# Performance work log

Hardware: AMD Instinct MI355X
Metric: run time of the kernel (lower is better)

Reference implementation:

```python
import jax, jax.numpy as jnp
import numpy as np

B, S, D, H = 2, 2048, 1024, 16
DK = D // H  # 64
ROPE_BASE = 10000.0


def _rope_tables(dk, seq_len, base=ROPE_BASE):
    inv_freq = 1.0 / base ** (jnp.arange(0, dk, 2, dtype=jnp.float32) / dk)
    t = jnp.arange(seq_len, dtype=jnp.float32)
    freqs = t[:, None] * inv_freq[None, :]            # [S, dk/2]
    cos = jnp.repeat(jnp.cos(freqs), 2, axis=-1)      # [S, dk] (repeat_interleave)
    sin = jnp.repeat(jnp.sin(freqs), 2, axis=-1)
    return cos, sin


def _rotate_half(x):
    x1, x2 = jnp.split(x, 2, axis=-1)
    return jnp.concatenate((-x2, x1), axis=-1)


def setup_inputs() -> dict:
    key = jax.random.key(0)
    ks = jax.random.split(key, 9)
    scale = 0.02
    x = jax.random.normal(ks[0], (B, S, D), jnp.float32)
    wq = jax.random.normal(ks[1], (D, D), jnp.float32) * scale
    wk = jax.random.normal(ks[2], (D, D), jnp.float32) * scale
    wv = jax.random.normal(ks[3], (D, D), jnp.float32) * scale
    wo = jax.random.normal(ks[4], (D, D), jnp.float32) * scale
    bq = jnp.zeros((D,), jnp.float32)
    bk = jnp.zeros((D,), jnp.float32)
    bv = jnp.zeros((D,), jnp.float32)
    bo = jnp.zeros((D,), jnp.float32)
    mask = jnp.tril(jnp.ones((S, S), dtype=bool))[None, None]  # [1,1,S,S] causal
    return {"x": x, "mask": mask, "wq": wq, "bq": bq, "wk": wk, "bk": bk,
            "wv": wv, "bv": bv, "wo": wo, "bo": bo}


def reference(x, mask, wq, bq, wk, bk, wv, bv, wo, bo):
    b, s, d = x.shape
    h, dk = H, DK
    # QKV projections (nn.Linear: x @ W^T + b), split heads -> [B,H,S,dk]
    q = (x @ wq.T + bq).reshape(b, s, h, dk).transpose(0, 2, 1, 3)
    k = (x @ wk.T + bk).reshape(b, s, h, dk).transpose(0, 2, 1, 3)
    v = (x @ wv.T + bv).reshape(b, s, h, dk).transpose(0, 2, 1, 3)
    # RoPE
    cos, sin = _rope_tables(dk, s)                    # [S, dk]
    cos = cos[None, None]                             # [1,1,S,dk]
    sin = sin[None, None]
    q = q * cos + _rotate_half(q) * sin
    k = k * cos + _rotate_half(k) * sin
    # Naive attention: full [B,H,S,S] scores
    scores = jnp.einsum("bhqd,bhkd->bhqk", q, k) / np.float32(np.sqrt(dk))
    scores = jnp.where(mask, scores, jnp.float32(-1e9))
    attn = jax.nn.softmax(scores, axis=-1)
    out = jnp.einsum("bhqk,bhkd->bhqd", attn, v)      # [B,H,S,dk]
    out = out.transpose(0, 2, 1, 3).reshape(b, s, d)  # [B,S,D]
    return out @ wo.T + bo
```

## Files before the change

### kernel.cpp

```cpp
#include <hip/hip_runtime.h>
#include <hip/hip_bf16.h>

#define B_ 2
#define S_ 2048
#define D_ 1024
#define H_ 16
#define DK_ 64
#define BH_ (B_*H_)

typedef __attribute__((ext_vector_type(8))) short short8;
typedef __attribute__((ext_vector_type(4))) short short4v;
typedef __attribute__((ext_vector_type(4))) float f32x4;

__device__ __forceinline__ unsigned short f2bf(float f) {
  unsigned u = __float_as_uint(f);
  u += 0x7FFFu + ((u >> 16) & 1u);
  return (unsigned short)(u >> 16);
}
__device__ __forceinline__ float bf2f(unsigned short b) {
  return __uint_as_float(((unsigned)b) << 16);
}
__device__ __forceinline__ unsigned pk2bf(float lo, float hi) {
  float2 f; f.x = lo; f.y = hi;
  __hip_bfloat162 t = __float22bfloat162_rn(f);
  unsigned r; __builtin_memcpy(&r, &t, 4); return r;
}

__global__ void cvt_kernel(const float* __restrict__ x, const float* __restrict__ wq,
                           const float* __restrict__ wk, const float* __restrict__ wv,
                           const float* __restrict__ wo, const float* __restrict__ bq,
                           const float* __restrict__ bk, const float* __restrict__ bv,
                           unsigned short* __restrict__ xb, unsigned short* __restrict__ wqkvb,
                           unsigned short* __restrict__ wob, float* __restrict__ bqkv) {
  long idx = ((long)blockIdx.x * blockDim.x + threadIdx.x) * 4;
  const long NX = (long)B_ * S_ * D_;
  const long NW = (long)D_ * D_;
  if (idx < NX) {
    float4 v = *(const float4*)(x + idx);
    short4v o; o[0] = f2bf(v.x); o[1] = f2bf(v.y); o[2] = f2bf(v.z); o[3] = f2bf(v.w);
    *(short4v*)(xb + idx) = o;
    return;
  }
  idx -= NX;
  if (idx < 3 * NW) {
    const float* w = (idx < NW) ? wq : ((idx < 2 * NW) ? wk : wv);
    float4 v = *(const float4*)(w + (idx & (NW - 1)));
    short4v o; o[0] = f2bf(v.x); o[1] = f2bf(v.y); o[2] = f2bf(v.z); o[3] = f2bf(v.w);
    *(short4v*)(wqkvb + idx) = o;
    return;
  }
  idx -= 3 * NW;
  if (idx < NW) {
    float4 v = *(const float4*)(wo + idx);
    short4v o; o[0] = f2bf(v.x); o[1] = f2bf(v.y); o[2] = f2bf(v.z); o[3] = f2bf(v.w);
    *(short4v*)(wob + idx) = o;
    return;
  }
  idx -= NW;
  if (idx < 3 * D_) {
    const float* bb = (idx < D_) ? (bq + idx) : ((idx < 2 * D_) ? (bk + idx - D_) : (bv + idx - 2 * D_));
    *(float4*)(bqkv + idx) = *(const float4*)bb;
  }
}

template<bool OUT_F32>
__global__ __launch_bounds__(256) void gemm_bt(const unsigned short* __restrict__ A,
                                               const unsigned short* __restrict__ Bm,
                                               const float* __restrict__ bias,
                                               void* __restrict__ Cp, int M, int N, int K) {
  __shared__ alignas(16) unsigned short As[128 * 32];
  __shared__ alignas(16) unsigned short Bs[128 * 32];
  const int t = threadIdx.x;
  const int w = t >> 6;
  const int lane = t & 63;
  const int brow = blockIdx.y * 128;
  const int bcol = blockIdx.x * 128;
  const int wr = (w >> 1) * 64, wc = (w & 1) * 64;
  const int lrow = t >> 2;
  const int lk = (t & 3) * 8;
  const int fr = lane & 15;
  const int fc = (lane >> 4) * 8;
  f32x4 acc[4][4] = {};

  for (int k0 = 0; k0 < K; k0 += 32) {
#pragma unroll
    for (int c = 0; c < 2; ++c) {
      const unsigned short* ga = A  + (long)(brow + c * 64 + lrow) * K + k0 + lk;
      const unsigned short* gb = Bm + (long)(bcol + c * 64 + lrow) * K + k0 + lk;
      unsigned short* la = As + (c * 64 + w * 16) * 32;
      unsigned short* lb = Bs + (c * 64 + w * 16) * 32;
      __builtin_amdgcn_global_load_lds((const __attribute__((address_space(1))) void*)ga,
                                       (__attribute__((address_space(3))) void*)la, 16, 0, 0);
      __builtin_amdgcn_global_load_lds((const __attribute__((address_space(1))) void*)gb,
                                       (__attribute__((address_space(3))) void*)lb, 16, 0, 0);
    }
    __syncthreads();
    short8 a[4], b[4];
#pragma unroll
    for (int m = 0; m < 4; ++m)
      a[m] = *(const short8*)(As + (wr + m * 16 + fr) * 32 + fc);
#pragma unroll
    for (int n = 0; n < 4; ++n)
      b[n] = *(const short8*)(Bs + (wc + n * 16 + fr) * 32 + fc);
#pragma unroll
    for (int m = 0; m < 4; ++m)
#pragma unroll
      for (int n = 0; n < 4; ++n)
        acc[m][n] = __builtin_amdgcn_mfma_f32_16x16x32_bf16(a[m], b[n], acc[m][n], 0, 0, 0);
    __syncthreads();
  }

  const int fg = lane >> 4;
#pragma unroll
  for (int m = 0; m < 4; ++m) {
#pragma unroll
    for (int n = 0; n < 4; ++n) {
      const int col = bcol + wc + n * 16 + fr;
      const float bv_ = bias[col];
#pragma unroll
      for (int i = 0; i < 4; ++i) {
        const int row = brow + wr + m * 16 + fg * 4 + i;
        const float v = acc[m][n][i] + bv_;
        if (OUT_F32) ((float*)Cp)[(long)row * N + col] = v;
        else ((unsigned short*)Cp)[(long)row * N + col] = f2bf(v);
      }
    }
  }
}

__global__ void rope_kernel(const unsigned short* __restrict__ qkv,
                            unsigned short* __restrict__ Qh,
                            unsigned short* __restrict__ Kf) {
  const int idx = blockIdx.x * blockDim.x + threadIdx.x;
  const int d = idx & 63;
  const int s = (idx >> 6) & (S_ - 1);
  const int bh = idx >> 17;
  const int b = bh >> 4, h = bh & 15;
  const long qrow = (long)(b * S_ + s) * 3072 + h * 64;
  const float qv = bf2f(qkv[qrow + d]);
  const float kv = bf2f(qkv[qrow + 1024 + d]);
  const int dp = (d < 32) ? d + 32 : d - 32;
  const float qp = bf2f(qkv[qrow + dp]);
  const float kp = bf2f(qkv[qrow + 1024 + dp]);
  const int j = d >> 1;
  const float invf = __expf(-(float)j * 0.28782313662425574f);
  const float fr = (float)s * invf;
  float sn, cs;
  __sincosf(fr, &sn, &cs);
  const float qo = (d < 32) ? (qv * cs - qp * sn) : (qv * cs + qp * sn);
  const float ko = (d < 32) ? (kv * cs - kp * sn) : (kv * cs + kp * sn);
  Qh[(long)bh * S_ * DK_ + (long)s * DK_ + d] = f2bf(qo * 0.125f);
  const long kfo = (long)bh * (S_ * DK_) + (long)(s >> 4) * 1024 +
                   (long)(d >> 5) * 512 + (long)((d >> 3) & 3) * 128 + (s & 15) * 8 + (d & 7);
  Kf[kfo] = f2bf(ko);
}

__global__ __launch_bounds__(256) void vtrans_kernel(const unsigned short* __restrict__ qkv,
                                                     unsigned short* __restrict__ Vf) {
  __shared__ unsigned short tile[32][72];
  const int bh = blockIdx.y;
  const int b = bh >> 4, h = bh & 15;
  const int c32 = blockIdx.x;
  const int tid = threadIdx.x;
  {
    const int r = tid >> 3, d0 = (tid & 7) * 8;
    *(short8*)&tile[r][d0] =
        *(const short8*)(qkv + (long)(b * S_ + c32 * 32 + r) * 3072 + 2048 + h * 64 + d0);
  }
  __syncthreads();
  const int t = tid >> 6, g = (tid >> 4) & 3, fr = tid & 15;
  short8 o;
#pragma unroll
  for (int j = 0; j < 8; ++j) {
    const int r = (j < 4) ? (4 * g + j) : (16 + 4 * g + (j - 4));
    o[j] = tile[r][t * 16 + fr];
  }
  *(short8*)(Vf + ((long)(bh * 64 + c32)) * 2048 + t * 512 + g * 128 + fr * 8) = o;
}

__global__ __launch_bounds__(256) void flash_kernel(const unsigned short* __restrict__ Qh,
                                                    const unsigned short* __restrict__ Kf,
                                                    const unsigned short* __restrict__ Vf,
                                                    unsigned short* __restrict__ attnout) {
  __shared__ alignas(16) unsigned short Ks[4096];
  __shared__ alignas(16) unsigned short Vs[4096];

  const int flat = (int)blockIdx.x;
  const int xcd = flat & 7;
  const int ix  = flat >> 3;
  const int k   = ix >> 5;
  const int c   = ix & 31;
  const int bh  = xcd * 4 + k;
  const int qblk = (k & 1) ? c : 31 - c;

  const int b = bh >> 4, h = bh & 15;
  const int w = threadIdx.x >> 6, lane = threadIdx.x & 63;
  const int fr = lane & 15, g = lane >> 4;
  const int qg = qblk * 64 + w * 16 + fr;

  const unsigned short* Qb = Qh + (long)bh * (S_ * DK_);
  const short8 qf0 = *(const short8*)(Qb + (long)qg * DK_ + g * 8);
  const short8 qf1 = *(const short8*)(Qb + (long)qg * DK_ + 32 + g * 8);

  short8 vone;
#pragma unroll
  for (int i = 0; i < 8; ++i) vone[i] = (short)0x3F80;

  f32x4 acc[4] = {};
  f32x4 acl = {};

  const unsigned short* kfb = Kf + (long)bh * (S_ * DK_);
  const unsigned short* vfb = Vf + (long)bh * (S_ * DK_);
  const int kvend = qblk * 64;
  const int frag = g * 128 + fr * 8;

  for (int kv0 = 0; kv0 <= kvend; kv0 += 64) {
    {
      const unsigned short* gk = kfb + (long)kv0 * 64 + w * 1024 + lane * 8;
      unsigned short* lk = Ks + w * 1024;
      __builtin_amdgcn_global_load_lds((const __attribute__((address_space(1))) void*)gk,
                                       (__attribute__((address_space(3))) void*)lk, 16, 0, 0);
      __builtin_amdgcn_global_load_lds((const __attribute__((address_space(1))) void*)(gk + 512),
                                       (__attribute__((address_space(3))) void*)(lk + 512), 16, 0, 0);
      const unsigned short* gv = vfb + (long)kv0 * 64 + w * 1024 + lane * 8;
      unsigned short* lv = Vs + w * 1024;
      __builtin_amdgcn_global_load_lds((const __attribute__((address_space(1))) void*)gv,
                                       (__attribute__((address_space(3))) void*)lv, 16, 0, 0);
      __builtin_amdgcn_global_load_lds((const __attribute__((address_space(1))) void*)(gv + 512),
                                       (__attribute__((address_space(3))) void*)(lv + 512), 16, 0, 0);
    }
    __syncthreads();

    f32x4 st[4];
    __builtin_amdgcn_s_setprio(1);
#pragma unroll
    for (int cc = 0; cc < 4; ++cc) {
      const short8 k0 = *(const short8*)(Ks + cc * 1024 + frag);
      const short8 k1 = *(const short8*)(Ks + cc * 1024 + 512 + frag);
      f32x4 z = {};
      z = __builtin_amdgcn_mfma_f32_16x16x32_bf16(k0, qf0, z, 0, 0, 0);
      z = __builtin_amdgcn_mfma_f32_16x16x32_bf16(k1, qf1, z, 0, 0, 0);
      st[cc] = z;
    }
    __builtin_amdgcn_s_setprio(0);

    float sv[16];
#pragma unroll
    for (int cc = 0; cc < 4; ++cc)
#pragma unroll
      for (int i = 0; i < 4; ++i) sv[cc * 4 + i] = st[cc][i];

    if (kv0 == kvend) {
#pragma unroll
      for (int cc = 0; cc < 4; ++cc)
#pragma unroll
        for (int i = 0; i < 4; ++i)
          if (cc * 16 + g * 4 + i > w * 16 + fr) sv[cc * 4 + i] = -3.0e38f;
    }

    float ps[16];
#pragma unroll
    for (int i = 0; i < 16; ++i) ps[i] = __expf(sv[i]);

    union { short8 s8; unsigned u[4]; } P0, P1;
#pragma unroll
    for (int i = 0; i < 4; ++i) {
      P0.u[i] = pk2bf(ps[2 * i], ps[2 * i + 1]);
      P1.u[i] = pk2bf(ps[8 + 2 * i], ps[8 + 2 * i + 1]);
    }

    __builtin_amdgcn_s_setprio(1);
#pragma unroll
    for (int t = 0; t < 4; ++t) {
      const short8 va = *(const short8*)(Vs + t * 512 + frag);
      const short8 vb = *(const short8*)(Vs + 2048 + t * 512 + frag);
      acc[t] = __builtin_amdgcn_mfma_f32_16x16x32_bf16(va, P0.s8, acc[t], 0, 0, 0);
      acc[t] = __builtin_amdgcn_mfma_f32_16x16x32_bf16(vb, P1.s8, acc[t], 0, 0, 0);
    }
    acl = __builtin_amdgcn_mfma_f32_16x16x32_bf16(vone, P0.s8, acl, 0, 0, 0);
    acl = __builtin_amdgcn_mfma_f32_16x16x32_bf16(vone, P1.s8, acl, 0, 0, 0);
    __builtin_amdgcn_s_setprio(0);
    __syncthreads();
  }

  const float ri = 1.0f / acl[0];
  const long orow = (long)(b * S_ + qg) * D_ + h * DK_;
#pragma unroll
  for (int t = 0; t < 4; ++t) {
    short4v ov;
#pragma unroll
    for (int i = 0; i < 4; ++i) ov[i] = (short)f2bf(acc[t][i] * ri);
    *(short4v*)(attnout + orow + t * 16 + g * 4) = ov;
  }
}

extern "C" void kernel_launch(void* const* d_in, const int* in_sizes, int n_in,
                              void* d_out, int out_size, void* d_ws, size_t ws_size,
                              hipStream_t stream) {
  const float* x  = (const float*)d_in[0];
  const float* wq = (const float*)d_in[2];
  const float* bq = (const float*)d_in[3];
  const float* wk = (const float*)d_in[4];
  const float* bk = (const float*)d_in[5];
  const float* wv = (const float*)d_in[6];
  const float* bv = (const float*)d_in[7];
  const float* wo = (const float*)d_in[8];
  const float* bo = (const float*)d_in[9];

  const long NX = (long)B_ * S_ * D_;
  const long NW = (long)D_ * D_;

  unsigned short* xb    = (unsigned short*)d_ws;
  unsigned short* wqkvb = xb + NX;
  unsigned short* wob   = wqkvb + 3 * NW;
  float*          bqkv  = (float*)(wob + NW);
  unsigned short* qkv   = (unsigned short*)(bqkv + 3 * D_);
  unsigned short* Qh    = qkv + (long)(B_ * S_) * 3 * D_;
  unsigned short* Kf    = Qh + NX;
  unsigned short* Vf    = Kf + NX;
  unsigned short* attnout = xb;

  const long ncvt4 = (NX + 3 * NW + NW + 3 * D_) / 4;
  cvt_kernel<<<(int)((ncvt4 + 255) / 256), 256, 0, stream>>>(x, wq, wk, wv, wo, bq, bk, bv,
                                                             xb, wqkvb, wob, bqkv);
  gemm_bt<false><<<dim3(24, 32), 256, 0, stream>>>(xb, wqkvb, bqkv, qkv, 4096, 3072, 1024);
  rope_kernel<<<(int)(NX / 256), 256, 0, stream>>>(qkv, Qh, Kf);
  vtrans_kernel<<<dim3(64, BH_), 256, 0, stream>>>(qkv, Vf);
  flash_kernel<<<1024, 256, 0, stream>>>(Qh, Kf, Vf, attnout);
  gemm_bt<true><<<dim3(8, 32), 256, 0, stream>>>(attnout, wob, bo, d_out, 4096, 1024, 1024);
}
```

Measured before the change: 126.7 us.

## Pre-tile GEMM operands into contiguous 128x32 blocks for conflict-free LDS loads

```diff
diff --git a/kernel.cpp b/kernel.cpp
--- a/kernel.cpp
+++ b/kernel.cpp
@@ -24,6 +24,10 @@
   float2 f; f.x = lo; f.y = hi;
   __hip_bfloat162 t = __float22bfloat162_rn(f);
   unsigned r; __builtin_memcpy(&r, &t, 4); return r;
+}
+
+__device__ __forceinline__ long ftile_off(int n, int k, int ktiles) {
+  return ((long)(n >> 7) * ktiles + (k >> 5)) * 4096 + ((k >> 3) & 3) * 1024 + (n & 127) * 8 + (k & 7);
 }
 
 __global__ void cvt_kernel(const float* __restrict__ x, const float* __restrict__ wq,
@@ -38,7 +42,8 @@
   if (idx < NX) {
     float4 v = *(const float4*)(x + idx);
     short4v o; o[0] = f2bf(v.x); o[1] = f2bf(v.y); o[2] = f2bf(v.z); o[3] = f2bf(v.w);
-    *(short4v*)(xb + idx) = o;
+    const int m = (int)(idx >> 10), k = (int)(idx & 1023);
+    *(short4v*)(xb + ftile_off(m, k, 32)) = o;
     return;
   }
   idx -= NX;
@@ -46,14 +51,16 @@
     const float* w = (idx < NW) ? wq : ((idx < 2 * NW) ? wk : wv);
     float4 v = *(const float4*)(w + (idx & (NW - 1)));
     short4v o; o[0] = f2bf(v.x); o[1] = f2bf(v.y); o[2] = f2bf(v.z); o[3] = f2bf(v.w);
-    *(short4v*)(wqkvb + idx) = o;
+    const int n = (int)(idx >> 10), k = (int)(idx & 1023);
+    *(short4v*)(wqkvb + ftile_off(n, k, 32)) = o;
     return;
   }
   idx -= 3 * NW;
   if (idx < NW) {
     float4 v = *(const float4*)(wo + idx);
     short4v o; o[0] = f2bf(v.x); o[1] = f2bf(v.y); o[2] = f2bf(v.z); o[3] = f2bf(v.w);
-    *(short4v*)(wob + idx) = o;
+    const int n = (int)(idx >> 10), k = (int)(idx & 1023);
+    *(short4v*)(wob + ftile_off(n, k, 32)) = o;
     return;
   }
   idx -= NW;
@@ -68,40 +75,38 @@
                                                const unsigned short* __restrict__ Bm,
                                                const float* __restrict__ bias,
                                                void* __restrict__ Cp, int M, int N, int K) {
-  __shared__ alignas(16) unsigned short As[128 * 32];
-  __shared__ alignas(16) unsigned short Bs[128 * 32];
+  __shared__ alignas(16) unsigned short As[4096];
+  __shared__ alignas(16) unsigned short Bs[4096];
   const int t = threadIdx.x;
   const int w = t >> 6;
   const int lane = t & 63;
   const int brow = blockIdx.y * 128;
   const int bcol = blockIdx.x * 128;
   const int wr = (w >> 1) * 64, wc = (w & 1) * 64;
-  const int lrow = t >> 2;
-  const int lk = (t & 3) * 8;
   const int fr = lane & 15;
-  const int fc = (lane >> 4) * 8;
+  const int g = lane >> 4;
+  const int ktiles = K >> 5;
   f32x4 acc[4][4] = {};
 
-  for (int k0 = 0; k0 < K; k0 += 32) {
-#pragma unroll
-    for (int c = 0; c < 2; ++c) {
-      const unsigned short* ga = A  + (long)(brow + c * 64 + lrow) * K + k0 + lk;
-      const unsigned short* gb = Bm + (long)(bcol + c * 64 + lrow) * K + k0 + lk;
-      unsigned short* la = As + (c * 64 + w * 16) * 32;
-      unsigned short* lb = Bs + (c * 64 + w * 16) * 32;
-      __builtin_amdgcn_global_load_lds((const __attribute__((address_space(1))) void*)ga,
-                                       (__attribute__((address_space(3))) void*)la, 16, 0, 0);
-      __builtin_amdgcn_global_load_lds((const __attribute__((address_space(1))) void*)gb,
-                                       (__attribute__((address_space(3))) void*)lb, 16, 0, 0);
+  for (int kt = 0; kt < ktiles; ++kt) {
+    const unsigned short* Asrc = A  + ((long)blockIdx.y * ktiles + kt) * 4096;
+    const unsigned short* Bsrc = Bm + ((long)blockIdx.x * ktiles + kt) * 4096;
+#pragma unroll
+    for (int j = 0; j < 2; ++j) {
+      const int off = (w * 2 + j) * 512;
+      __builtin_amdgcn_global_load_lds((const __attribute__((address_space(1))) void*)(Asrc + off + lane * 8),
+                                       (__attribute__((address_space(3))) void*)(As + off), 16, 0, 0);
+      __builtin_amdgcn_global_load_lds((const __attribute__((address_space(1))) void*)(Bsrc + off + lane * 8),
+                                       (__attribute__((address_space(3))) void*)(Bs + off), 16, 0, 0);
     }
     __syncthreads();
     short8 a[4], b[4];
 #pragma unroll
     for (int m = 0; m < 4; ++m)
-      a[m] = *(const short8*)(As + (wr + m * 16 + fr) * 32 + fc);
+      a[m] = *(const short8*)(As + g * 1024 + (wr + m * 16 + fr) * 8);
 #pragma unroll
     for (int n = 0; n < 4; ++n)
-      b[n] = *(const short8*)(Bs + (wc + n * 16 + fr) * 32 + fc);
+      b[n] = *(const short8*)(Bs + g * 1024 + (wc + n * 16 + fr) * 8);
 #pragma unroll
     for (int m = 0; m < 4; ++m)
 #pragma unroll
@@ -110,7 +115,7 @@
     __syncthreads();
   }
 
-  const int fg = lane >> 4;
+  const int fg = g;
 #pragma unroll
   for (int m = 0; m < 4; ++m) {
 #pragma unroll
@@ -284,13 +289,14 @@
   }
 
   const float ri = 1.0f / acl[0];
-  const long orow = (long)(b * S_ + qg) * D_ + h * DK_;
+  const int row = b * S_ + qg;
 #pragma unroll
   for (int t = 0; t < 4; ++t) {
     short4v ov;
 #pragma unroll
     for (int i = 0; i < 4; ++i) ov[i] = (short)f2bf(acc[t][i] * ri);
-    *(short4v*)(attnout + orow + t * 16 + g * 4) = ov;
+    const int kcol = h * 64 + t * 16 + g * 4;
+    *(short4v*)(attnout + ftile_off(row, kcol, 32)) = ov;
   }
 }
 
```

Measured after the change: 133.5 us. 5.4% more time.
